# Optimization experiments

Hardware: AMD Instinct MI355X
Metric: run time of the kernel (lower is better)

Reference implementation:

```python
import jax, jax.numpy as jnp
import numpy as np

N_NODES = 50000
N_EDGES = 800000
VOCAB = 100000
EMB = 64
HID = 64
N_CLASSES = 10
N_GRAPHS = 512


def setup_inputs() -> dict:
    key = jax.random.key(0)
    ks = jax.random.split(key, 12)
    node_ids = jax.random.randint(ks[0], (N_NODES,), 0, VOCAB)
    edge_index = jax.random.randint(ks[1], (2, N_EDGES), 0, N_NODES)
    batch = jnp.sort(jax.random.randint(ks[2], (N_NODES,), 0, N_GRAPHS))
    emb = jax.random.normal(ks[3], (VOCAB, EMB), jnp.float32)
    s_e = 1.0 / np.sqrt(EMB)
    s_h = 1.0 / np.sqrt(HID)
    Wl0 = jax.random.normal(ks[4], (EMB, HID), jnp.float32) * s_e
    bl0 = jnp.zeros((HID,), jnp.float32)
    Wr0 = jax.random.normal(ks[5], (EMB, HID), jnp.float32) * s_e
    Wl1 = jax.random.normal(ks[6], (HID, HID), jnp.float32) * s_h
    bl1 = jnp.zeros((HID,), jnp.float32)
    Wr1 = jax.random.normal(ks[7], (HID, HID), jnp.float32) * s_h
    Wout = jax.random.normal(ks[8], (HID, N_CLASSES), jnp.float32) * s_h
    bout = jnp.zeros((N_CLASSES,), jnp.float32)
    return {"node_ids": node_ids, "edge_index": edge_index, "batch": batch,
            "emb": emb, "Wl0": Wl0, "bl0": bl0, "Wr0": Wr0,
            "Wl1": Wl1, "bl1": bl1, "Wr1": Wr1, "Wout": Wout, "bout": bout}


def _sage_conv(x, src, dst, Wl, bl, Wr):
    # PyG SAGEConv (aggr='mean'): out_i = lin_l(mean_{j in N(i)} x_j) + lin_r(x_i)
    msg = x[src]                                      # [E, d] gather
    s = jax.ops.segment_sum(msg, dst, num_segments=N_NODES)
    cnt = jax.ops.segment_sum(jnp.ones((msg.shape[0], 1), x.dtype), dst,
                              num_segments=N_NODES)
    mean = jnp.where(cnt > 0, s / jnp.maximum(cnt, 1), 0)
    return mean @ Wl + bl + x @ Wr


def reference(node_ids, edge_index, batch, emb, Wl0, bl0, Wr0, Wl1, bl1, Wr1, Wout, bout):
    x = emb[node_ids]                                  # [N, EMB]
    src, dst = edge_index[0], edge_index[1]
    x = jax.nn.relu(_sage_conv(x, src, dst, Wl0, bl0, Wr0))
    x = jax.nn.relu(_sage_conv(x, src, dst, Wl1, bl1, Wr1))
    # global_mean_pool over graph ids
    s = jax.ops.segment_sum(x, batch, num_segments=N_GRAPHS)
    cnt = jax.ops.segment_sum(jnp.ones((x.shape[0], 1), x.dtype), batch,
                              num_segments=N_GRAPHS)
    pooled = jnp.where(cnt > 0, s / jnp.maximum(cnt, 1), 0)   # [G, HID]
    return pooled @ Wout + bout                        # [G, N_CLASSES]
```

## Files before the change

kernel.cpp:

```cpp
#include <hip/hip_runtime.h>
#include <hip/hip_bf16.h>

#define N_NODES 50000
#define N_EDGES 800000
#define EMB 64
#define HID 64
#define N_CLASSES 10
#define N_GRAPHS 512

#define BKT_SHIFT 6
#define BKT_NODES 64
#define NB_BKT ((N_NODES + BKT_NODES - 1) / BKT_NODES)
#define BKT_CAP 1408
#define EB_CHUNK 8192
#define EB_BLOCKS ((N_EDGES + EB_CHUNK - 1) / EB_CHUNK)
#define XFORM_BLOCKS ((N_NODES + 63) / 64)
#define XPAD 68
#define POOL_SPAN 66

#define ACC8(vv, A)                                                            \
    do {                                                                       \
        A[0] += __uint_as_float((vv).x << 16);                                 \
        A[1] += __uint_as_float((vv).x & 0xFFFF0000u);                         \
        A[2] += __uint_as_float((vv).y << 16);                                 \
        A[3] += __uint_as_float((vv).y & 0xFFFF0000u);                         \
        A[4] += __uint_as_float((vv).z << 16);                                 \
        A[5] += __uint_as_float((vv).z & 0xFFFF0000u);                         \
        A[6] += __uint_as_float((vv).w << 16);                                 \
        A[7] += __uint_as_float((vv).w & 0xFFFF0000u);                         \
    } while (0)

__device__ __forceinline__ void build_local_csr(
    int bucket, const int* __restrict__ cnt, const int* __restrict__ ebuf,
    unsigned short* lcsr, int* nhist, int* sval, int* sexcl, int* ncur) {
    int tid = threadIdx.x;
    int bs = bucket * BKT_CAP;
    int ne = min(cnt[bucket], BKT_CAP);
    if (tid < BKT_NODES) { nhist[tid] = 0; ncur[tid] = 0; }
    __syncthreads();
    for (int i = tid; i < ne; i += 256)
        atomicAdd(&nhist[ebuf[bs + i] >> 16], 1);
    __syncthreads();
    if (tid < BKT_NODES) sval[tid] = nhist[tid];
    __syncthreads();
    for (int off = 1; off < BKT_NODES; off <<= 1) {
        int t = 0;
        if (tid < BKT_NODES && tid >= off) t = nhist[tid - off];
        __syncthreads();
        if (tid < BKT_NODES) nhist[tid] += t;
        __syncthreads();
    }
    if (tid < BKT_NODES) sexcl[tid] = nhist[tid] - sval[tid];
    __syncthreads();
    for (int i = tid; i < ne; i += 256) {
        int p = ebuf[bs + i];
        int l = p >> 16;
        int r = atomicAdd(&ncur[l], 1);
        lcsr[sexcl[l] + r] = (unsigned short)(p & 0xFFFF);
    }
    __syncthreads();
}

__device__ __forceinline__ void agg_node8(
    int s0, int deg, int sl,
    const unsigned short* lcsr,
    const __hip_bfloat16* __restrict__ Pb,
    float out[8]) {
    float a[4][8];
#pragma unroll
    for (int i = 0; i < 4; i++)
#pragma unroll
        for (int j = 0; j < 8; j++) a[i][j] = 0.f;
    int s1 = s0 + deg;
    for (int base = s0; base < s1; base += 8) {
        int c = min(8, s1 - base);
        if (c == 8) {
            int n0 = lcsr[base + 0];
            int n1 = lcsr[base + 1];
            int n2 = lcsr[base + 2];
            int n3 = lcsr[base + 3];
            int n4 = lcsr[base + 4];
            int n5 = lcsr[base + 5];
            int n6 = lcsr[base + 6];
            int n7 = lcsr[base + 7];
            uint4 v0 = ((const uint4*)(Pb + (size_t)n0 * 64))[sl];
            uint4 v1 = ((const uint4*)(Pb + (size_t)n1 * 64))[sl];
            uint4 v2 = ((const uint4*)(Pb + (size_t)n2 * 64))[sl];
            uint4 v3 = ((const uint4*)(Pb + (size_t)n3 * 64))[sl];
            uint4 v4 = ((const uint4*)(Pb + (size_t)n4 * 64))[sl];
            uint4 v5 = ((const uint4*)(Pb + (size_t)n5 * 64))[sl];
            uint4 v6 = ((const uint4*)(Pb + (size_t)n6 * 64))[sl];
            uint4 v7 = ((const uint4*)(Pb + (size_t)n7 * 64))[sl];
            ACC8(v0, a[0]); ACC8(v1, a[1]); ACC8(v2, a[2]); ACC8(v3, a[3]);
            ACC8(v4, a[0]); ACC8(v5, a[1]); ACC8(v6, a[2]); ACC8(v7, a[3]);
        } else {
            for (int j = 0; j < c; j++) {
                int n = lcsr[base + j];
                uint4 v = ((const uint4*)(Pb + (size_t)n * 64))[sl];
                ACC8(v, a[j & 3]);
            }
        }
    }
    float inv = (deg > 0) ? 1.0f / (float)deg : 0.0f;
#pragma unroll
    for (int j = 0; j < 8; j++)
        out[j] = (a[0][j] + a[1][j] + a[2][j] + a[3][j]) * inv;
}

__global__ __launch_bounds__(256) void k_combo(
    const int* __restrict__ esrc, const int* __restrict__ edst,
    int* __restrict__ cnt, int* __restrict__ ebuf,
    const int* __restrict__ ids, const float* __restrict__ emb,
    const float* __restrict__ Wl, const float* __restrict__ bl,
    const float* __restrict__ Wr,
    __hip_bfloat16* __restrict__ Pb, float* __restrict__ Qout) {
    __shared__ float sW[64 * 64];
    __shared__ float sX[64 * XPAD];
    int t = threadIdx.x;
    if (blockIdx.x < EB_BLOCKS) {
        int* h = (int*)sW;
        int* bbase = h + NB_BKT;
        int* cur = (int*)sX;
        for (int i = t; i < NB_BKT; i += 256) { h[i] = 0; cur[i] = 0; }
        __syncthreads();
        int base = blockIdx.x * EB_CHUNK;
        int end = min(base + EB_CHUNK, N_EDGES);
        for (int i = base + t; i < end; i += 256)
            atomicAdd(&h[edst[i] >> BKT_SHIFT], 1);
        __syncthreads();
        for (int i = t; i < NB_BKT; i += 256)
            if (h[i]) bbase[i] = i * BKT_CAP + atomicAdd(&cnt[i], h[i]);
        __syncthreads();
        for (int i = base + t; i < end; i += 256) {
            int d = edst[i], s = esrc[i];
            int b = d >> BKT_SHIFT;
            int r = atomicAdd(&cur[b], 1);
            int slot = bbase[b] + r;
            if (slot < (b + 1) * BKT_CAP)
                ebuf[slot] = ((d & (BKT_NODES - 1)) << 16) | s;
        }
        return;
    }
    int tile = (blockIdx.x - EB_BLOCKS) * 64;
    for (int i = t; i < 64 * 16; i += 256)
        ((float4*)sW)[i] = ((const float4*)Wl)[i];
    for (int i = t; i < 64 * 16; i += 256) {
        int r = i >> 4, c = i & 15;
        int node = tile + r;
        float4 v = make_float4(0.f, 0.f, 0.f, 0.f);
        if (node < N_NODES)
            v = ((const float4*)(emb + (size_t)ids[node] * 64))[c];
        *(float4*)&sX[r * XPAD + c * 4] = v;
    }
    __syncthreads();
    int dg = t & 15, ng = t >> 4;
    float acc[4][4];
#pragma unroll
    for (int i = 0; i < 4; i++)
#pragma unroll
        for (int j = 0; j < 4; j++) acc[i][j] = 0.f;
#pragma unroll 4
    for (int k = 0; k < 64; k++) {
        float4 w = *(const float4*)&sW[k * 64 + dg * 4];
#pragma unroll
        for (int i = 0; i < 4; i++) {
            float xv = sX[(ng + i * 16) * XPAD + k];
            acc[i][0] = fmaf(xv, w.x, acc[i][0]);
            acc[i][1] = fmaf(xv, w.y, acc[i][1]);
            acc[i][2] = fmaf(xv, w.z, acc[i][2]);
            acc[i][3] = fmaf(xv, w.w, acc[i][3]);
        }
    }
#pragma unroll
    for (int i = 0; i < 4; i++) {
        int node = tile + ng + i * 16;
        if (node < N_NODES) {
            union { ushort4 u; __hip_bfloat16 h[4]; } pk;
            pk.h[0] = __float2bfloat16(acc[i][0]);
            pk.h[1] = __float2bfloat16(acc[i][1]);
            pk.h[2] = __float2bfloat16(acc[i][2]);
            pk.h[3] = __float2bfloat16(acc[i][3]);
            *(ushort4*)&Pb[(size_t)node * 64 + dg * 4] = pk.u;
        }
    }
    __syncthreads();
    for (int i = t; i < 64 * 16; i += 256)
        ((float4*)sW)[i] = ((const float4*)Wr)[i];
    __syncthreads();
#pragma unroll
    for (int i = 0; i < 4; i++)
#pragma unroll
        for (int j = 0; j < 4; j++) acc[i][j] = 0.f;
#pragma unroll 4
    for (int k = 0; k < 64; k++) {
        float4 w = *(const float4*)&sW[k * 64 + dg * 4];
#pragma unroll
        for (int i = 0; i < 4; i++) {
            float xv = sX[(ng + i * 16) * XPAD + k];
            acc[i][0] = fmaf(xv, w.x, acc[i][0]);
            acc[i][1] = fmaf(xv, w.y, acc[i][1]);
            acc[i][2] = fmaf(xv, w.z, acc[i][2]);
            acc[i][3] = fmaf(xv, w.w, acc[i][3]);
        }
    }
    float4 blv = *(const float4*)&bl[dg * 4];
#pragma unroll
    for (int i = 0; i < 4; i++) {
        int node = tile + ng + i * 16;
        if (node < N_NODES)
            *(float4*)&Qout[(size_t)node * 64 + dg * 4] =
                make_float4(acc[i][0] + blv.x, acc[i][1] + blv.y,
                            acc[i][2] + blv.z, acc[i][3] + blv.w);
    }
}

__global__ __launch_bounds__(256) void k_fused1(
    const int* __restrict__ cnt, const int* __restrict__ ebuf,
    const __hip_bfloat16* __restrict__ Pb0, const float* __restrict__ Wl,
    const float* __restrict__ bl, const float* __restrict__ Wr,
    __hip_bfloat16* __restrict__ Pb1, float* __restrict__ H) {
    __shared__ float sW[64 * 64];
    __shared__ float sX[64 * XPAD];
    __shared__ unsigned short lcsr[BKT_CAP];
    __shared__ int nhist[BKT_NODES], sval[BKT_NODES], sexcl[BKT_NODES], ncur[BKT_NODES];
    int t = threadIdx.x;
    int tile = blockIdx.x * 64;
    for (int i = t; i < 64 * 16; i += 256)
        ((float4*)sW)[i] = ((const float4*)Wl)[i];
    build_local_csr(blockIdx.x, cnt, ebuf, lcsr, nhist, sval, sexcl, ncur);
    int grp = t >> 3, sl = t & 7;
    for (int nn = 0; nn < 2; nn++) {
        int ln = grp * 2 + nn;
        int node = tile + ln;
        float m[8];
        agg_node8(sexcl[ln], sval[ln], sl, lcsr, Pb0, m);
        if (node < N_NODES) {
            size_t off = (size_t)node * 64 + sl * 8;
            float4 q0 = *(const float4*)&H[off];
            float4 q1 = *(const float4*)&H[off + 4];
            m[0] = fmaxf(m[0] + q0.x, 0.f);
            m[1] = fmaxf(m[1] + q0.y, 0.f);
            m[2] = fmaxf(m[2] + q0.z, 0.f);
            m[3] = fmaxf(m[3] + q0.w, 0.f);
            m[4] = fmaxf(m[4] + q1.x, 0.f);
            m[5] = fmaxf(m[5] + q1.y, 0.f);
            m[6] = fmaxf(m[6] + q1.z, 0.f);
            m[7] = fmaxf(m[7] + q1.w, 0.f);
        } else {
#pragma unroll
            for (int j = 0; j < 8; j++) m[j] = 0.f;
        }
        *(float4*)&sX[ln * XPAD + sl * 8] = make_float4(m[0], m[1], m[2], m[3]);
        *(float4*)&sX[ln * XPAD + sl * 8 + 4] = make_float4(m[4], m[5], m[6], m[7]);
    }
    __syncthreads();
    int dg = t & 15, ng = t >> 4;
    float acc[4][4];
#pragma unroll
    for (int i = 0; i < 4; i++)
#pragma unroll
        for (int j = 0; j < 4; j++) acc[i][j] = 0.f;
#pragma unroll 4
    for (int k = 0; k < 64; k++) {
        float4 w = *(const float4*)&sW[k * 64 + dg * 4];
#pragma unroll
        for (int i = 0; i < 4; i++) {
            float xv = sX[(ng + i * 16) * XPAD + k];
            acc[i][0] = fmaf(xv, w.x, acc[i][0]);
            acc[i][1] = fmaf(xv, w.y, acc[i][1]);
            acc[i][2] = fmaf(xv, w.z, acc[i][2]);
            acc[i][3] = fmaf(xv, w.w, acc[i][3]);
        }
    }
#pragma unroll
    for (int i = 0; i < 4; i++) {
        int node = tile + ng + i * 16;
        if (node < N_NODES) {
            union { ushort4 u; __hip_bfloat16 h[4]; } pk;
            pk.h[0] = __float2bfloat16(acc[i][0]);
            pk.h[1] = __float2bfloat16(acc[i][1]);
            pk.h[2] = __float2bfloat16(acc[i][2]);
            pk.h[3] = __float2bfloat16(acc[i][3]);
            *(ushort4*)&Pb1[(size_t)node * 64 + dg * 4] = pk.u;
        }
    }
    __syncthreads();
    for (int i = t; i < 64 * 16; i += 256)
        ((float4*)sW)[i] = ((const float4*)Wr)[i];
    __syncthreads();
#pragma unroll
    for (int i = 0; i < 4; i++)
#pragma unroll
        for (int j = 0; j < 4; j++) acc[i][j] = 0.f;
#pragma unroll 4
    for (int k = 0; k < 64; k++) {
        float4 w = *(const float4*)&sW[k * 64 + dg * 4];
#pragma unroll
        for (int i = 0; i < 4; i++) {
            float xv = sX[(ng + i * 16) * XPAD + k];
            acc[i][0] = fmaf(xv, w.x, acc[i][0]);
            acc[i][1] = fmaf(xv, w.y, acc[i][1]);
            acc[i][2] = fmaf(xv, w.z, acc[i][2]);
            acc[i][3] = fmaf(xv, w.w, acc[i][3]);
        }
    }
    float4 blv = *(const float4*)&bl[dg * 4];
#pragma unroll
    for (int i = 0; i < 4; i++) {
        int node = tile + ng + i * 16;
        if (node < N_NODES)
            *(float4*)&H[(size_t)node * 64 + dg * 4] =
                make_float4(acc[i][0] + blv.x, acc[i][1] + blv.y,
                            acc[i][2] + blv.z, acc[i][3] + blv.w);
    }
}

__global__ __launch_bounds__(256) void k_agg2_pool(
    const int* __restrict__ cnt, const int* __restrict__ ebuf,
    const __hip_bfloat16* __restrict__ Pb, const float* __restrict__ H,
    const int* __restrict__ batch, float* __restrict__ psum) {
    __shared__ float acc[POOL_SPAN * 64];
    __shared__ unsigned short lcsr[BKT_CAP];
    __shared__ int nhist[BKT_NODES], sval[BKT_NODES], sexcl[BKT_NODES], ncur[BKT_NODES];
    int t = threadIdx.x;
    int nb = blockIdx.x * 64;
    for (int i = t; i < POOL_SPAN * 64; i += 256) acc[i] = 0.f;
    build_local_csr(blockIdx.x, cnt, ebuf, lcsr, nhist, sval, sexcl, ncur);
    int gmin = batch[nb];
    int grp = t >> 3, sl = t & 7;
    for (int nn = 0; nn < 2; nn++) {
        int ln = grp * 2 + nn;
        int node = nb + ln;
        float m[8];
        agg_node8(sexcl[ln], sval[ln], sl, lcsr, Pb, m);
        if (node < N_NODES) {
            size_t off = (size_t)node * 64 + sl * 8;
            float4 q0 = *(const float4*)&H[off];
            float4 q1 = *(const float4*)&H[off + 4];
            m[0] = fmaxf(m[0] + q0.x, 0.f);
            m[1] = fmaxf(m[1] + q0.y, 0.f);
            m[2] = fmaxf(m[2] + q0.z, 0.f);
            m[3] = fmaxf(m[3] + q0.w, 0.f);
            m[4] = fmaxf(m[4] + q1.x, 0.f);
            m[5] = fmaxf(m[5] + q1.y, 0.f);
            m[6] = fmaxf(m[6] + q1.z, 0.f);
            m[7] = fmaxf(m[7] + q1.w, 0.f);
            int g = batch[node];
            int lg = g - gmin;
            if (lg < POOL_SPAN) {
#pragma unroll
                for (int j = 0; j < 8; j++)
                    atomicAdd(&acc[lg * 64 + sl * 8 + j], m[j]);
            } else {
#pragma unroll
                for (int j = 0; j < 8; j++)
                    atomicAdd(&psum[(size_t)g * 64 + sl * 8 + j], m[j]);
            }
        }
    }
    __syncthreads();
    int nlast = min(nb + 63, N_NODES - 1);
    int gspan = min(batch[nlast] - gmin + 1, POOL_SPAN);
    for (int i = t; i < gspan * 64; i += 256) {
        float v = acc[i];
        if (v != 0.f)
            atomicAdd(&psum[(size_t)(gmin + (i >> 6)) * 64 + (i & 63)], v);
    }
}

__device__ __forceinline__ int lower_bound_batch(const int* __restrict__ batch, int val) {
    int lo = 0, hi = N_NODES;
    while (lo < hi) {
        int mid = (lo + hi) >> 1;
        if (batch[mid] < val) lo = mid + 1; else hi = mid;
    }
    return lo;
}

__global__ __launch_bounds__(256) void k_out(
    const int* __restrict__ batch, const float* __restrict__ psum,
    const float* __restrict__ Wout, const float* __restrict__ bout,
    float* __restrict__ out) {
    int w = threadIdx.x >> 6, lane = threadIdx.x & 63;
    int g = blockIdx.x * 4 + w;
    if (g >= N_GRAPHS) return;
    int s0 = lower_bound_batch(batch, g);
    int s1 = lower_bound_batch(batch, g + 1);
    int cntg = s1 - s0;
    float inv = (cntg > 0) ? 1.0f / (float)cntg : 0.0f;
    float pooled = psum[(size_t)g * 64 + lane] * inv;
#pragma unroll
    for (int c = 0; c < N_CLASSES; c++) {
        float v = pooled * Wout[lane * N_CLASSES + c];
#pragma unroll
        for (int off = 32; off > 0; off >>= 1) v += __shfl_down(v, off, 64);
        if (lane == 0) out[(size_t)g * N_CLASSES + c] = v + bout[c];
    }
}


extern "C" void kernel_launch(void* const* d_in, const int* in_sizes, int n_in,
                              void* d_out, int out_size, void* d_ws, size_t ws_size,
                              hipStream_t stream) {
    const int*   node_ids = (const int*)d_in[0];
    const int*   edge_idx = (const int*)d_in[1];
    const int*   batch    = (const int*)d_in[2];
    const float* emb      = (const float*)d_in[3];
    const float* Wl0      = (const float*)d_in[4];
    const float* bl0      = (const float*)d_in[5];
    const float* Wr0      = (const float*)d_in[6];
    const float* Wl1      = (const float*)d_in[7];
    const float* bl1      = (const float*)d_in[8];
    const float* Wr1      = (const float*)d_in[9];
    const float* Wout     = (const float*)d_in[10];
    const float* bout     = (const float*)d_in[11];
    float* out = (float*)d_out;

    const int* esrc = edge_idx;
    const int* edst = edge_idx + N_EDGES;

    __hip_bfloat16* Pb0 = (__hip_bfloat16*)d_ws;
    __hip_bfloat16* Pb1 = Pb0 + (size_t)N_NODES * 64;
    float* H = (float*)(Pb1 + (size_t)N_NODES * 64);
    int* ebuf = (int*)(H + (size_t)N_NODES * 64);
    int* cnt = ebuf + (size_t)NB_BKT * BKT_CAP;
    float* psum = (float*)(cnt + NB_BKT);

    const int BLK = 256;

    hipMemsetAsync(cnt, 0, (NB_BKT + N_GRAPHS * 64) * sizeof(int), stream);

    k_combo<<<EB_BLOCKS + XFORM_BLOCKS, BLK, 0, stream>>>(
        esrc, edst, cnt, ebuf, node_ids, emb, Wl0, bl0, Wr0, Pb0, H);

    k_fused1<<<XFORM_BLOCKS, BLK, 0, stream>>>(cnt, ebuf, Pb0, Wl1, bl1, Wr1, Pb1, H);

    k_agg2_pool<<<NB_BKT, BLK, 0, stream>>>(cnt, ebuf, Pb1, H, batch, psum);

    k_out<<<(N_GRAPHS + 3) / 4, BLK, 0, stream>>>(batch, psum, Wout, bout, out);
}
```

Before: 222.7 us.

## Halve bucket/tile size to 32 nodes and fuse both GEMMs reading weights from global

Shrinks the destination-bucket and node-tile size from 64 to 32, so each of 256 threads aggregates a single node and twice as many blocks are launched. The Wl and Wr transforms are merged into one loop that reads weights directly from global/L1 instead of staging them in shared memory, which removes two syncs and about 16KB of LDS per block. Bucket capacity and the pooling span are cut to match. The aim is more blocks in flight and higher occupancy for the latency-bound gathers, at the cost of more global weight loads, a larger bucket histogram in the edge-bucketing pass, and a tighter bucket-overflow margin.

```diff
diff --git a/kernel.cpp b/kernel.cpp
--- a/kernel.cpp
+++ b/kernel.cpp
@@ -8,15 +8,15 @@
 #define N_CLASSES 10
 #define N_GRAPHS 512
 
-#define BKT_SHIFT 6
-#define BKT_NODES 64
+#define BKT_SHIFT 5
+#define BKT_NODES 32
 #define NB_BKT ((N_NODES + BKT_NODES - 1) / BKT_NODES)
-#define BKT_CAP 1408
+#define BKT_CAP 800
 #define EB_CHUNK 8192
 #define EB_BLOCKS ((N_EDGES + EB_CHUNK - 1) / EB_CHUNK)
-#define XFORM_BLOCKS ((N_NODES + 63) / 64)
+#define XFORM_BLOCKS NB_BKT
 #define XPAD 68
-#define POOL_SPAN 66
+#define POOL_SPAN 6
 
 #define ACC8(vv, A)                                                            \
     do {                                                                       \
@@ -107,6 +107,52 @@
         out[j] = (a[0][j] + a[1][j] + a[2][j] + a[3][j]) * inv;
 }
 
+__device__ __forceinline__ void tile_gemm32(
+    const float* sX, const float* __restrict__ Wl, const float* __restrict__ bl,
+    const float* __restrict__ Wr, int tile,
+    __hip_bfloat16* __restrict__ PbOut, float* __restrict__ QOut) {
+    int t = threadIdx.x;
+    int dg = t & 15, ng = t >> 4;
+    float accL[2][4], accR[2][4];
+#pragma unroll
+    for (int i = 0; i < 2; i++)
+#pragma unroll
+        for (int j = 0; j < 4; j++) { accL[i][j] = 0.f; accR[i][j] = 0.f; }
+#pragma unroll 4
+    for (int k = 0; k < 64; k++) {
+        float4 wl = ((const float4*)Wl)[k * 16 + dg];
+        float4 wr = ((const float4*)Wr)[k * 16 + dg];
+#pragma unroll
+        for (int i = 0; i < 2; i++) {
+            float xv = sX[(ng + i * 16) * XPAD + k];
+            accL[i][0] = fmaf(xv, wl.x, accL[i][0]);
+            accL[i][1] = fmaf(xv, wl.y, accL[i][1]);
+            accL[i][2] = fmaf(xv, wl.z, accL[i][2]);
+            accL[i][3] = fmaf(xv, wl.w, accL[i][3]);
+            accR[i][0] = fmaf(xv, wr.x, accR[i][0]);
+            accR[i][1] = fmaf(xv, wr.y, accR[i][1]);
+            accR[i][2] = fmaf(xv, wr.z, accR[i][2]);
+            accR[i][3] = fmaf(xv, wr.w, accR[i][3]);
+        }
+    }
+    float4 blv = *(const float4*)&bl[dg * 4];
+#pragma unroll
+    for (int i = 0; i < 2; i++) {
+        int node = tile + ng + i * 16;
+        if (node < N_NODES) {
+            union { ushort4 u; __hip_bfloat16 h[4]; } pk;
+            pk.h[0] = __float2bfloat16(accL[i][0]);
+            pk.h[1] = __float2bfloat16(accL[i][1]);
+            pk.h[2] = __float2bfloat16(accL[i][2]);
+            pk.h[3] = __float2bfloat16(accL[i][3]);
+            *(ushort4*)&PbOut[(size_t)node * 64 + dg * 4] = pk.u;
+            *(float4*)&QOut[(size_t)node * 64 + dg * 4] =
+                make_float4(accR[i][0] + blv.x, accR[i][1] + blv.y,
+                            accR[i][2] + blv.z, accR[i][3] + blv.w);
+        }
+    }
+}
+
 __global__ __launch_bounds__(256) void k_combo(
     const int* __restrict__ esrc, const int* __restrict__ edst,
     int* __restrict__ cnt, int* __restrict__ ebuf,
@@ -114,13 +160,12 @@
     const float* __restrict__ Wl, const float* __restrict__ bl,
     const float* __restrict__ Wr,
     __hip_bfloat16* __restrict__ Pb, float* __restrict__ Qout) {
-    __shared__ float sW[64 * 64];
-    __shared__ float sX[64 * XPAD];
+    __shared__ int smem[3 * NB_BKT > 32 * XPAD ? 3 * NB_BKT : 32 * XPAD];
     int t = threadIdx.x;
     if (blockIdx.x < EB_BLOCKS) {
-        int* h = (int*)sW;
+        int* h = smem;
         int* bbase = h + NB_BKT;
-        int* cur = (int*)sX;
+        int* cur = bbase + NB_BKT;
         for (int i = t; i < NB_BKT; i += 256) { h[i] = 0; cur[i] = 0; }
         __syncthreads();
         int base = blockIdx.x * EB_CHUNK;
@@ -141,10 +186,9 @@
         }
         return;
     }
-    int tile = (blockIdx.x - EB_BLOCKS) * 64;
-    for (int i = t; i < 64 * 16; i += 256)
-        ((float4*)sW)[i] = ((const float4*)Wl)[i];
-    for (int i = t; i < 64 * 16; i += 256) {
+    float* sX = (float*)smem;
+    int tile = (blockIdx.x - EB_BLOCKS) * 32;
+    for (int i = t; i < 32 * 16; i += 256) {
         int r = i >> 4, c = i & 15;
         int node = tile + r;
         float4 v = make_float4(0.f, 0.f, 0.f, 0.f);
@@ -153,65 +197,7 @@
         *(float4*)&sX[r * XPAD + c * 4] = v;
     }
     __syncthreads();
-    int dg = t & 15, ng = t >> 4;
-    float acc[4][4];
-#pragma unroll
-    for (int i = 0; i < 4; i++)
-#pragma unroll
-        for (int j = 0; j < 4; j++) acc[i][j] = 0.f;
-#pragma unroll 4
-    for (int k = 0; k < 64; k++) {
-        float4 w = *(const float4*)&sW[k * 64 + dg * 4];
-#pragma unroll
-        for (int i = 0; i < 4; i++) {
-            float xv = sX[(ng + i * 16) * XPAD + k];
-            acc[i][0] = fmaf(xv, w.x, acc[i][0]);
-            acc[i][1] = fmaf(xv, w.y, acc[i][1]);
-            acc[i][2] = fmaf(xv, w.z, acc[i][2]);
-            acc[i][3] = fmaf(xv, w.w, acc[i][3]);
-        }
-    }
-#pragma unroll
-    for (int i = 0; i < 4; i++) {
-        int node = tile + ng + i * 16;
-        if (node < N_NODES) {
-            union { ushort4 u; __hip_bfloat16 h[4]; } pk;
-            pk.h[0] = __float2bfloat16(acc[i][0]);
-            pk.h[1] = __float2bfloat16(acc[i][1]);
-            pk.h[2] = __float2bfloat16(acc[i][2]);
-            pk.h[3] = __float2bfloat16(acc[i][3]);
-            *(ushort4*)&Pb[(size_t)node * 64 + dg * 4] = pk.u;
-        }
-    }
-    __syncthreads();
-    for (int i = t; i < 64 * 16; i += 256)
-        ((float4*)sW)[i] = ((const float4*)Wr)[i];
-    __syncthreads();
-#pragma unroll
-    for (int i = 0; i < 4; i++)
-#pragma unroll
-        for (int j = 0; j < 4; j++) acc[i][j] = 0.f;
-#pragma unroll 4
-    for (int k = 0; k < 64; k++) {
-        float4 w = *(const float4*)&sW[k * 64 + dg * 4];
-#pragma unroll
-        for (int i = 0; i < 4; i++) {
-            float xv = sX[(ng + i * 16) * XPAD + k];
-            acc[i][0] = fmaf(xv, w.x, acc[i][0]);
-            acc[i][1] = fmaf(xv, w.y, acc[i][1]);
-            acc[i][2] = fmaf(xv, w.z, acc[i][2]);
-            acc[i][3] = fmaf(xv, w.w, acc[i][3]);
-        }
-    }
-    float4 blv = *(const float4*)&bl[dg * 4];
-#pragma unroll
-    for (int i = 0; i < 4; i++) {
-        int node = tile + ng + i * 16;
-        if (node < N_NODES)
-            *(float4*)&Qout[(size_t)node * 64 + dg * 4] =
-                make_float4(acc[i][0] + blv.x, acc[i][1] + blv.y,
-                            acc[i][2] + blv.z, acc[i][3] + blv.w);
-    }
+    tile_gemm32(sX, Wl, bl, Wr, tile, Pb, Qout);
 }
 
 __global__ __launch_bounds__(256) void k_fused1(
@@ -219,18 +205,14 @@
     const __hip_bfloat16* __restrict__ Pb0, const float* __restrict__ Wl,
     const float* __restrict__ bl, const float* __restrict__ Wr,
     __hip_bfloat16* __restrict__ Pb1, float* __restrict__ H) {
-    __shared__ float sW[64 * 64];
-    __shared__ float sX[64 * XPAD];
+    __shared__ float sX[32 * XPAD];
     __shared__ unsigned short lcsr[BKT_CAP];
     __shared__ int nhist[BKT_NODES], sval[BKT_NODES], sexcl[BKT_NODES], ncur[BKT_NODES];
     int t = threadIdx.x;
-    int tile = blockIdx.x * 64;
-    for (int i = t; i < 64 * 16; i += 256)
-        ((float4*)sW)[i] = ((const float4*)Wl)[i];
+    int tile = blockIdx.x * 32;
     build_local_csr(blockIdx.x, cnt, ebuf, lcsr, nhist, sval, sexcl, ncur);
-    int grp = t >> 3, sl = t & 7;
-    for (int nn = 0; nn < 2; nn++) {
-        int ln = grp * 2 + nn;
+    int ln = t >> 3, sl = t & 7;
+    {
         int node = tile + ln;
         float m[8];
         agg_node8(sexcl[ln], sval[ln], sl, lcsr, Pb0, m);
@@ -254,65 +236,7 @@
         *(float4*)&sX[ln * XPAD + sl * 8 + 4] = make_float4(m[4], m[5], m[6], m[7]);
     }
     __syncthreads();
-    int dg = t & 15, ng = t >> 4;
-    float acc[4][4];
-#pragma unroll
-    for (int i = 0; i < 4; i++)
-#pragma unroll
-        for (int j = 0; j < 4; j++) acc[i][j] = 0.f;
-#pragma unroll 4
-    for (int k = 0; k < 64; k++) {
-        float4 w = *(const float4*)&sW[k * 64 + dg * 4];
-#pragma unroll
-        for (int i = 0; i < 4; i++) {
-            float xv = sX[(ng + i * 16) * XPAD + k];
-            acc[i][0] = fmaf(xv, w.x, acc[i][0]);
-            acc[i][1] = fmaf(xv, w.y, acc[i][1]);
-            acc[i][2] = fmaf(xv, w.z, acc[i][2]);
-            acc[i][3] = fmaf(xv, w.w, acc[i][3]);
-        }
-    }
-#pragma unroll
-    for (int i = 0; i < 4; i++) {
-        int node = tile + ng + i * 16;
-        if (node < N_NODES) {
-            union { ushort4 u; __hip_bfloat16 h[4]; } pk;
-            pk.h[0] = __float2bfloat16(acc[i][0]);
-            pk.h[1] = __float2bfloat16(acc[i][1]);
-            pk.h[2] = __float2bfloat16(acc[i][2]);
-            pk.h[3] = __float2bfloat16(acc[i][3]);
-            *(ushort4*)&Pb1[(size_t)node * 64 + dg * 4] = pk.u;
-        }
-    }
-    __syncthreads();
-    for (int i = t; i < 64 * 16; i += 256)
-        ((float4*)sW)[i] = ((const float4*)Wr)[i];
-    __syncthreads();
-#pragma unroll
-    for (int i = 0; i < 4; i++)
-#pragma unroll
-        for (int j = 0; j < 4; j++) acc[i][j] = 0.f;
-#pragma unroll 4
-    for (int k = 0; k < 64; k++) {
-        float4 w = *(const float4*)&sW[k * 64 + dg * 4];
-#pragma unroll
-        for (int i = 0; i < 4; i++) {
-            float xv = sX[(ng + i * 16) * XPAD + k];
-            acc[i][0] = fmaf(xv, w.x, acc[i][0]);
-            acc[i][1] = fmaf(xv, w.y, acc[i][1]);
-            acc[i][2] = fmaf(xv, w.z, acc[i][2]);
-            acc[i][3] = fmaf(xv, w.w, acc[i][3]);
-        }
-    }
-    float4 blv = *(const float4*)&bl[dg * 4];
-#pragma unroll
-    for (int i = 0; i < 4; i++) {
-        int node = tile + ng + i * 16;
-        if (node < N_NODES)
-            *(float4*)&H[(size_t)node * 64 + dg * 4] =
-                make_float4(acc[i][0] + blv.x, acc[i][1] + blv.y,
-                            acc[i][2] + blv.z, acc[i][3] + blv.w);
-    }
+    tile_gemm32(sX, Wl, bl, Wr, tile, Pb1, H);
 }
 
 __global__ __launch_bounds__(256) void k_agg2_pool(
@@ -323,13 +247,12 @@
     __shared__ unsigned short lcsr[BKT_CAP];
     __shared__ int nhist[BKT_NODES], sval[BKT_NODES], sexcl[BKT_NODES], ncur[BKT_NODES];
     int t = threadIdx.x;
-    int nb = blockIdx.x * 64;
+    int nb = blockIdx.x * 32;
     for (int i = t; i < POOL_SPAN * 64; i += 256) acc[i] = 0.f;
     build_local_csr(blockIdx.x, cnt, ebuf, lcsr, nhist, sval, sexcl, ncur);
     int gmin = batch[nb];
-    int grp = t >> 3, sl = t & 7;
-    for (int nn = 0; nn < 2; nn++) {
-        int ln = grp * 2 + nn;
+    int ln = t >> 3, sl = t & 7;
+    {
         int node = nb + ln;
         float m[8];
         agg_node8(sexcl[ln], sval[ln], sl, lcsr, Pb, m);
@@ -359,7 +282,7 @@
         }
     }
     __syncthreads();
-    int nlast = min(nb + 63, N_NODES - 1);
+    int nlast = min(nb + 31, N_NODES - 1);
     int gspan = min(batch[nlast] - gmin + 1, POOL_SPAN);
     for (int i = t; i < gspan * 64; i += 256) {
         float v = acc[i];
```

Measured after the change: 239.5 us. 1.08x slower.
